# Optimization experiments

Hardware: AMD Instinct MI355X
Metric: run time of the kernel (lower is better)

## Reference

```python
import jax, jax.numpy as jnp
import numpy as np

N = 50000   # nodes
E = 800000  # edges
IN_DIM = 512
HID = 256   # total hidden (4 heads x 64)
HEADS = 4
OUT_DIM = 256
NEG_SLOPE = 0.2


def setup_inputs() -> dict:
    key = jax.random.key(0)
    ks = jax.random.split(key, 16)
    s = 0.05
    d = {
        "feats": jax.random.normal(ks[0], (N, IN_DIM), jnp.float32),
        "src": jax.random.randint(ks[1], (E,), 0, N, jnp.int32),
        "dst": jax.random.randint(ks[2], (E,), 0, N, jnp.int32),
        # layer 0: in 512 -> 4 heads x 64
        "W0": jax.random.normal(ks[3], (IN_DIM, HID), jnp.float32) * s,
        "al0": jax.random.normal(ks[4], (HEADS, HID // HEADS), jnp.float32) * s,
        "ar0": jax.random.normal(ks[5], (HEADS, HID // HEADS), jnp.float32) * s,
        "b0": jnp.zeros((HID,), jnp.float32),
        # layer 1: in 256 -> 4 heads x 64
        "W1": jax.random.normal(ks[6], (HID, HID), jnp.float32) * s,
        "al1": jax.random.normal(ks[7], (HEADS, HID // HEADS), jnp.float32) * s,
        "ar1": jax.random.normal(ks[8], (HEADS, HID // HEADS), jnp.float32) * s,
        "b1": jnp.zeros((HID,), jnp.float32),
        # layer 2: in 256 -> 1 head x 256, no activation
        "W2": jax.random.normal(ks[9], (HID, OUT_DIM), jnp.float32) * s,
        "al2": jax.random.normal(ks[10], (1, OUT_DIM), jnp.float32) * s,
        "ar2": jax.random.normal(ks[11], (1, OUT_DIM), jnp.float32) * s,
        "b2": jnp.zeros((OUT_DIM,), jnp.float32),
    }
    return d


def gat_conv(h, src, dst, W, al, ar, b, act):
    """DGL-style GATConv (no dropout, no residual). Returns [N, H, D]."""
    H, D = al.shape
    feat = (h @ W).reshape(-1, H, D)                       # [N,H,D]
    el = jnp.einsum('nhd,hd->nh', feat, al)                # [N,H]
    er = jnp.einsum('nhd,hd->nh', feat, ar)                # [N,H]
    e = jax.nn.leaky_relu(el[src] + er[dst], NEG_SLOPE)    # [E,H]
    # edge softmax over incoming edges per destination node
    m = jax.ops.segment_max(e, dst, num_segments=N)        # [N,H]
    ex = jnp.exp(e - m[dst])                               # [E,H]
    s = jax.ops.segment_sum(ex, dst, num_segments=N)       # [N,H]
    alpha = ex / s[dst]                                    # [E,H]
    msg = jax.ops.segment_sum(alpha[:, :, None] * feat[src], dst, num_segments=N)  # [N,H,D]
    out = msg + b.reshape(1, H, D)
    return act(out) if act is not None else out


def reference(feats, src, dst, W0, al0, ar0, b0, W1, al1, ar1, b1, W2, al2, ar2, b2):
    h = gat_conv(feats, src, dst, W0, al0, ar0, b0, jax.nn.relu)
    h = h.reshape(h.shape[0], -1)                          # flatten heads
    h = gat_conv(h, src, dst, W1, al1, ar1, b1, jax.nn.relu)
    h = h.reshape(h.shape[0], -1)
    h = gat_conv(h, src, dst, W2, al2, ar2, b2, None)
    h = h.mean(axis=1)                                     # last layer: mean over (single) head
    return h
```

## Files before the change

### kernel.cpp

```cpp
#include <hip/hip_runtime.h>
#include <hip/hip_bf16.h>
#include <math.h>


#define HID 256

typedef __attribute__((ext_vector_type(8))) __bf16 bf16x8;
typedef __attribute__((ext_vector_type(4))) __bf16 bf16x4;
typedef __attribute__((ext_vector_type(8))) _Float16 half8;
typedef __attribute__((ext_vector_type(4))) _Float16 half4;
typedef __attribute__((ext_vector_type(4))) float floatx4;

__device__ __forceinline__ void gl_lds16(const void* g, void* l) {
    __builtin_amdgcn_global_load_lds(
        (const __attribute__((address_space(1))) void*)g,
        (__attribute__((address_space(3))) void*)l, 16, 0, 0);
}


__global__ void hist_kernel(const int* __restrict__ dst, int* __restrict__ cnt, int E) {
    int e = blockIdx.x * blockDim.x + threadIdx.x;
    if (e < E) atomicAdd(&cnt[dst[e]], 1);
}

__global__ __launch_bounds__(256) void scan1_kernel(const int* __restrict__ cnt,
                                                    int* __restrict__ bsum, int n) {
    __shared__ int w[4];
    int t = threadIdx.x;
    int i = blockIdx.x * 256 + t;
    int c = (i < n) ? cnt[i] : 0;
    int acc = c;
#pragma unroll
    for (int off = 32; off > 0; off >>= 1) acc += __shfl_xor(acc, off);
    if ((t & 63) == 0) w[t >> 6] = acc;
    __syncthreads();
    if (t == 0) bsum[blockIdx.x] = w[0] + w[1] + w[2] + w[3];
}

__global__ __launch_bounds__(256) void scan2_kernel(const int* __restrict__ bsum,
                                                    int* __restrict__ boff, int nb) {
    __shared__ int buf[256];
    int t = threadIdx.x;
    int v = (t < nb) ? bsum[t] : 0;
    buf[t] = v;
    __syncthreads();
    for (int off = 1; off < 256; off <<= 1) {
        int x = (t >= off) ? buf[t - off] : 0;
        __syncthreads();
        buf[t] += x;
        __syncthreads();
    }
    if (t < nb) boff[t] = buf[t] - v;
}

__global__ __launch_bounds__(256) void scan3_kernel(const int* __restrict__ cnt,
                                                    const int* __restrict__ boff,
                                                    int* __restrict__ rowptr,
                                                    int* __restrict__ cursor, int n) {
    __shared__ int buf[256];
    int t = threadIdx.x;
    int i = blockIdx.x * 256 + t;
    int c = (i < n) ? cnt[i] : 0;
    buf[t] = c;
    __syncthreads();
    for (int off = 1; off < 256; off <<= 1) {
        int x = (t >= off) ? buf[t - off] : 0;
        __syncthreads();
        buf[t] += x;
        __syncthreads();
    }
    int start = boff[blockIdx.x] + buf[t] - c;
    if (i < n) {
        rowptr[i] = start;
        cursor[i] = start;
        if (i == n - 1) rowptr[n] = start + c;
    }
}

__global__ void fill_kernel(const int* __restrict__ src, const int* __restrict__ dst,
                            int* __restrict__ cursor, int* __restrict__ adj, int E) {
    int e = blockIdx.x * blockDim.x + threadIdx.x;
    if (e < E) {
        int d = dst[e];
        int pos = atomicAdd(&cursor[d], 1);
        adj[pos] = src[e];
    }
}


__device__ __forceinline__ void splitT_one(const float* W, __bf16* ht, __bf16* lt,
                                           int idx, int K) {
    int k = idx >> 8, n = idx & 255;
    float v = W[idx];
    __bf16 h = (__bf16)v;
    ht[(size_t)n * K + k] = h;
    lt[(size_t)n * K + k] = (__bf16)(v - (float)h);
}

__global__ __launch_bounds__(256) void splitT_all_kernel(
    const float* __restrict__ W0, const float* __restrict__ W1,
    const float* __restrict__ W2, __bf16* h0, __bf16* l0, __bf16* h1,
    __bf16* l1, __bf16* h2, __bf16* l2) {
    int i = blockIdx.x * 256 + threadIdx.x;
    const int n0 = 512 * 256, n1 = 256 * 256;
    if (i < n0) splitT_one(W0, h0, l0, i, 512);
    else if (i < n0 + n1) splitT_one(W1, h1, l1, i - n0, 256);
    else if (i < n0 + 2 * n1) splitT_one(W2, h2, l2, i - n0 - n1, 256);
}


template <bool SPLITA>
__global__ __launch_bounds__(256, 2) void gemm_mfma_kernel(
    const float* __restrict__ Af, const __bf16* __restrict__ Ah,
    const __bf16* __restrict__ Al, const __bf16* __restrict__ Bht,
    const __bf16* __restrict__ Blt, _Float16* __restrict__ C,
    const float* __restrict__ al, const float* __restrict__ ar,
    float* __restrict__ el, float* __restrict__ er, int M, int K, int H) {
    __shared__ __bf16 sAh[128 * 32];
    __shared__ __bf16 sAl[128 * 32];
    __shared__ __bf16 sBh[128 * 32];
    __shared__ __bf16 sBl[128 * 32];

    int t = threadIdx.x;
    int wave = t >> 6, lane = t & 63;
    int wr = wave >> 1, wc = wave & 1;
    int quad = lane >> 4, m16 = lane & 15;

    int rowA0 = blockIdx.y * 128;
    int rowB0 = blockIdx.x * 128;

    int sr = t >> 2;
    int ke = (t & 3) * 8;
    int ldso = t * 8;
    int srow = t >> 1;
    int kb = (t & 1) * 16;

    size_t ar0 = 0, ar1 = 0, af0 = 0;
    if (SPLITA) {
        af0 = (size_t)min(rowA0 + srow, M - 1) * K + kb;
    } else {
        ar0 = (size_t)min(rowA0 + sr, M - 1) * K;
        ar1 = (size_t)min(rowA0 + sr + 64, M - 1) * K;
    }
    size_t br0 = (size_t)(rowB0 + sr) * K;
    size_t br1 = (size_t)(rowB0 + sr + 64) * K;

    floatx4 acc[4][4];
    floatx4 z = {0.f, 0.f, 0.f, 0.f};
#pragma unroll
    for (int i = 0; i < 4; i++)
#pragma unroll
        for (int j = 0; j < 4; j++) acc[i][j] = z;

    int nk = K >> 5;
    for (int kt = 0; kt < nk; kt++) {
        int k0s = (kt << 5) + ke;
        gl_lds16(Bht + br0 + k0s, &sBh[ldso]);
        gl_lds16(Bht + br1 + k0s, &sBh[2048 + ldso]);
        gl_lds16(Blt + br0 + k0s, &sBl[ldso]);
        gl_lds16(Blt + br1 + k0s, &sBl[2048 + ldso]);
        if (SPLITA) {
            const float* ap = Af + af0 + (kt << 5);
            float4 v0 = ((const float4*)ap)[0];
            float4 v1 = ((const float4*)ap)[1];
            float4 v2 = ((const float4*)ap)[2];
            float4 v3 = ((const float4*)ap)[3];
            float vv[16] = {v0.x, v0.y, v0.z, v0.w, v1.x, v1.y, v1.z, v1.w,
                            v2.x, v2.y, v2.z, v2.w, v3.x, v3.y, v3.z, v3.w};
            bf16x8 h0, h1, l0, l1;
#pragma unroll
            for (int c = 0; c < 8; c++) {
                __bf16 hv = (__bf16)vv[c];
                h0[c] = hv;
                l0[c] = (__bf16)(vv[c] - (float)hv);
                __bf16 hv2 = (__bf16)vv[8 + c];
                h1[c] = hv2;
                l1[c] = (__bf16)(vv[8 + c] - (float)hv2);
            }
            int so = srow * 32 + kb;
            *(bf16x8*)&sAh[so] = h0;
            *(bf16x8*)&sAh[so + 8] = h1;
            *(bf16x8*)&sAl[so] = l0;
            *(bf16x8*)&sAl[so + 8] = l1;
        } else {
            gl_lds16(Ah + ar0 + k0s, &sAh[ldso]);
            gl_lds16(Ah + ar1 + k0s, &sAh[2048 + ldso]);
            gl_lds16(Al + ar0 + k0s, &sAl[ldso]);
            gl_lds16(Al + ar1 + k0s, &sAl[2048 + ldso]);
        }
        __syncthreads();

        bf16x8 fah[4], fal[4], fbh[4], fbl[4];
#pragma unroll
        for (int i = 0; i < 4; i++) {
            int off = (wr * 64 + i * 16 + m16) * 32 + quad * 8;
            fah[i] = *(const bf16x8*)&sAh[off];
            fal[i] = *(const bf16x8*)&sAl[off];
        }
#pragma unroll
        for (int j = 0; j < 4; j++) {
            int off = (wc * 64 + j * 16 + m16) * 32 + quad * 8;
            fbh[j] = *(const bf16x8*)&sBh[off];
            fbl[j] = *(const bf16x8*)&sBl[off];
        }
#pragma unroll
        for (int i = 0; i < 4; i++)
#pragma unroll
            for (int j = 0; j < 4; j++) {
                acc[i][j] = __builtin_amdgcn_mfma_f32_16x16x32_bf16(fah[i], fbh[j], acc[i][j], 0, 0, 0);
                acc[i][j] = __builtin_amdgcn_mfma_f32_16x16x32_bf16(fah[i], fbl[j], acc[i][j], 0, 0, 0);
                acc[i][j] = __builtin_amdgcn_mfma_f32_16x16x32_bf16(fal[i], fbh[j], acc[i][j], 0, 0, 0);
            }
        __syncthreads();
    }

#pragma unroll
    for (int i = 0; i < 4; i++) {
        int rowb = rowA0 + wr * 64 + i * 16 + quad * 4;
#pragma unroll
        for (int j = 0; j < 4; j++) {
            int col = rowB0 + wc * 64 + j * 16 + m16;
#pragma unroll
            for (int r = 0; r < 4; r++) {
                int row = rowb + r;
                if (row < M) C[(size_t)row * HID + col] = (_Float16)acc[i][j][r];
            }
        }
    }

    float alv[4], arv[4];
#pragma unroll
    for (int j = 0; j < 4; j++) {
        int col = rowB0 + wc * 64 + j * 16 + m16;
        alv[j] = al[col];
        arv[j] = ar[col];
    }
    int h = ((rowB0 + wc * 64) >> 6) & (H - 1);
#pragma unroll
    for (int i = 0; i < 4; i++) {
        int rowb = rowA0 + wr * 64 + i * 16 + quad * 4;
#pragma unroll
        for (int r = 0; r < 4; r++) {
            float pe = acc[i][0][r] * alv[0] + acc[i][1][r] * alv[1] +
                       acc[i][2][r] * alv[2] + acc[i][3][r] * alv[3];
            float pr = acc[i][0][r] * arv[0] + acc[i][1][r] * arv[1] +
                       acc[i][2][r] * arv[2] + acc[i][3][r] * arv[3];
#pragma unroll
            for (int off = 1; off < 16; off <<= 1) {
                pe += __shfl_xor(pe, off);
                pr += __shfl_xor(pr, off);
            }
            int row = rowb + r;
            if (m16 == 0 && row < M) {
                if (H == 4) {
                    el[row * 4 + h] = pe;
                    er[row * 4 + h] = pr;
                } else {
                    atomicAdd(&el[row], pe);
                    atomicAdd(&er[row], pr);
                }
            }
        }
    }
}


__global__ __launch_bounds__(256) void gemm_kernel(const float* __restrict__ A,
                                                   const float* __restrict__ B,
                                                   _Float16* __restrict__ C,
                                                   int M, int K, int Nn) {
    __shared__ float As[16][128];
    __shared__ float Bs[16][128];

    int t = threadIdx.x;
    int tx = t & 15, ty = t >> 4;
    int arow = t >> 1;
    int acol = (t & 1) * 8;
    int brow = t >> 4;
    int bcol = (t & 15) * 8;

    int gArow = blockIdx.y * 128 + arow;
    const float* aPtr = A + (size_t)gArow * K + acol;
    const float* bPtr = B + (size_t)brow * Nn + blockIdx.x * 128 + bcol;

    float acc[8][8];
#pragma unroll
    for (int i = 0; i < 8; i++)
#pragma unroll
        for (int j = 0; j < 8; j++) acc[i][j] = 0.f;

    bool aok = (gArow < M);
    int nk = K >> 4;
    for (int kt = 0; kt < nk; kt++) {
        int k0 = kt << 4;
        float4 av0 = make_float4(0.f, 0.f, 0.f, 0.f), av1 = av0;
        if (aok) {
            av0 = *(const float4*)(aPtr + k0);
            av1 = *(const float4*)(aPtr + k0 + 4);
        }
        float4 bv0 = *(const float4*)(bPtr + (size_t)k0 * Nn);
        float4 bv1 = *(const float4*)(bPtr + (size_t)k0 * Nn + 4);

        As[acol + 0][arow] = av0.x;
        As[acol + 1][arow] = av0.y;
        As[acol + 2][arow] = av0.z;
        As[acol + 3][arow] = av0.w;
        As[acol + 4][arow] = av1.x;
        As[acol + 5][arow] = av1.y;
        As[acol + 6][arow] = av1.z;
        As[acol + 7][arow] = av1.w;
        *(float4*)&Bs[brow][bcol] = bv0;
        *(float4*)&Bs[brow][bcol + 4] = bv1;
        __syncthreads();

#pragma unroll
        for (int kk = 0; kk < 16; kk++) {
            float4 a0 = *(const float4*)&As[kk][ty * 4];
            float4 a1 = *(const float4*)&As[kk][64 + ty * 4];
            float4 b0 = *(const float4*)&Bs[kk][tx * 4];
            float4 b1 = *(const float4*)&Bs[kk][64 + tx * 4];
            float a[8] = {a0.x, a0.y, a0.z, a0.w, a1.x, a1.y, a1.z, a1.w};
            float b[8] = {b0.x, b0.y, b0.z, b0.w, b1.x, b1.y, b1.z, b1.w};
#pragma unroll
            for (int i = 0; i < 8; i++)
#pragma unroll
                for (int j = 0; j < 8; j++) acc[i][j] = fmaf(a[i], b[j], acc[i][j]);
        }
        __syncthreads();
    }

    int c0 = blockIdx.x * 128 + tx * 4;
#pragma unroll
    for (int half = 0; half < 2; half++) {
#pragma unroll
        for (int i = 0; i < 4; i++) {
            int r = blockIdx.y * 128 + half * 64 + ty * 4 + i;
            if (r < M) {
                _Float16* cp = C + (size_t)r * Nn + c0;
                int ai = half * 4 + i;
#pragma unroll
                for (int j = 0; j < 4; j++) {
                    cp[j] = (_Float16)acc[ai][j];
                    cp[64 + j] = (_Float16)acc[ai][4 + j];
                }
            }
        }
    }
}


__global__ __launch_bounds__(256) void elr_kernel(const _Float16* __restrict__ feat,
                                                  const float* __restrict__ al,
                                                  const float* __restrict__ ar,
                                                  float* __restrict__ el,
                                                  float* __restrict__ er, int H) {
    int n = blockIdx.x, t = threadIdx.x;
    float f = (float)feat[(size_t)n * HID + t];
    float a = f * al[t];
    float b = f * ar[t];
#pragma unroll
    for (int off = 32; off > 0; off >>= 1) {
        a += __shfl_xor(a, off);
        b += __shfl_xor(b, off);
    }
    __shared__ float pa[4], pb[4];
    int wave = t >> 6, lane = t & 63;
    if (lane == 0) { pa[wave] = a; pb[wave] = b; }
    __syncthreads();
    if (H == 4) {
        if (t < 4) {
            el[n * 4 + t] = pa[t];
            er[n * 4 + t] = pb[t];
        }
    } else {
        if (t == 0) {
            el[n] = pa[0] + pa[1] + pa[2] + pa[3];
            er[n] = pb[0] + pb[1] + pb[2] + pb[3];
        }
    }
}


template <int H, bool RELU, bool WF32, bool WSPLIT>
__global__ __launch_bounds__(256) void agg_tpl(
    const _Float16* __restrict__ feat, const float* __restrict__ el,
    const float* __restrict__ er, const int* __restrict__ rowptr,
    const int* __restrict__ adj, const float* __restrict__ bias,
    float* __restrict__ outf, __bf16* __restrict__ oh, __bf16* __restrict__ ol,
    int N) {
    int wave = threadIdx.x >> 6, lane = threadIdx.x & 63;
    int v = blockIdx.x * 4 + wave;
    if (v >= N) return;
    int row0 = rowptr[v];
    int deg = rowptr[v + 1] - row0;

    int l32 = lane & 31;
    int half = lane >> 5;
    int hd = (H == 4) ? (l32 >> 3) : 0;
    int d0 = l32 * 8;

    float o[8];
    if (deg > 0) {
        float er_h = (H == 4) ? er[v * 4 + hd] : er[v];
        const int* adjr = adj + row0;

        float a[8];
#pragma unroll
        for (int j = 0; j < 8; j++) a[j] = 0.f;
        float sl = 0.f;

        int e = 0;
        for (; e + 16 <= deg; e += 16) {
            int u[8];
            half8 f[8];
            float elv[8];
#pragma unroll
            for (int q = 0; q < 8; q++) u[q] = adjr[e + q * 2 + half];
#pragma unroll
            for (int q = 0; q < 8; q++)
                f[q] = *(const half8*)&feat[(size_t)u[q] * HID + d0];
#pragma unroll
            for (int q = 0; q < 8; q++)
                elv[q] = (H == 4) ? el[u[q] * 4 + hd] : el[u[q]];
#pragma unroll
            for (int q = 0; q < 8; q++) {
                float sc = elv[q] + er_h;
                sc = (sc > 0.f) ? sc : 0.2f * sc;
                float ex = __expf(sc);
                sl += ex;
#pragma unroll
                for (int j = 0; j < 8; j++) a[j] = fmaf(ex, (float)f[q][j], a[j]);
            }
        }
        for (; e + 8 <= deg; e += 8) {
            int u[4];
            half8 f[4];
            float elv[4];
#pragma unroll
            for (int q = 0; q < 4; q++) u[q] = adjr[e + q * 2 + half];
#pragma unroll
            for (int q = 0; q < 4; q++)
                f[q] = *(const half8*)&feat[(size_t)u[q] * HID + d0];
#pragma unroll
            for (int q = 0; q < 4; q++)
                elv[q] = (H == 4) ? el[u[q] * 4 + hd] : el[u[q]];
#pragma unroll
            for (int q = 0; q < 4; q++) {
                float sc = elv[q] + er_h;
                sc = (sc > 0.f) ? sc : 0.2f * sc;
                float ex = __expf(sc);
                sl += ex;
#pragma unroll
                for (int j = 0; j < 8; j++) a[j] = fmaf(ex, (float)f[q][j], a[j]);
            }
        }
        for (; e < deg; e += 2) {
            int ee = e + half;
            bool act = ee < deg;
            int es = act ? ee : (deg - 1);
            int u = adjr[es];
            float elvq = (H == 4) ? el[u * 4 + hd] : el[u];
            half8 f = *(const half8*)&feat[(size_t)u * HID + d0];
            float sc = elvq + er_h;
            sc = (sc > 0.f) ? sc : 0.2f * sc;
            float ex = act ? __expf(sc) : 0.f;
            sl += ex;
#pragma unroll
            for (int j = 0; j < 8; j++) a[j] = fmaf(ex, (float)f[j], a[j]);
        }

#pragma unroll
        for (int j = 0; j < 8; j++) a[j] += __shfl_xor(a[j], 32);
        sl += __shfl_xor(sl, 32);
        float inv = 1.f / sl;

#pragma unroll
        for (int j = 0; j < 8; j++) {
            o[j] = fmaf(a[j], inv, bias[d0 + j]);
            if (RELU) o[j] = fmaxf(o[j], 0.f);
        }
    } else {
#pragma unroll
        for (int j = 0; j < 8; j++) {
            o[j] = bias[d0 + j];
            if (RELU) o[j] = fmaxf(o[j], 0.f);
        }
    }

    if (half == 0) {
        size_t base = (size_t)v * HID + d0;
        if (WF32) {
            *(float4*)&outf[base] = make_float4(o[0], o[1], o[2], o[3]);
            *(float4*)&outf[base + 4] = make_float4(o[4], o[5], o[6], o[7]);
        }
        if (WSPLIT) {
            bf16x8 hh, ll;
#pragma unroll
            for (int j = 0; j < 8; j++) {
                __bf16 hv = (__bf16)o[j];
                hh[j] = hv;
                ll[j] = (__bf16)(o[j] - (float)hv);
            }
            *(bf16x8*)&oh[base] = hh;
            *(bf16x8*)&ol[base] = ll;
        }
    }
}


extern "C" void kernel_launch(void* const* d_in, const int* in_sizes, int n_in,
                              void* d_out, int out_size, void* d_ws, size_t ws_size,
                              hipStream_t stream) {
    const float* feats = (const float*)d_in[0];
    const int* src = (const int*)d_in[1];
    const int* dst = (const int*)d_in[2];
    const float* W0 = (const float*)d_in[3];
    const float* al0 = (const float*)d_in[4];
    const float* ar0 = (const float*)d_in[5];
    const float* b0 = (const float*)d_in[6];
    const float* W1 = (const float*)d_in[7];
    const float* al1 = (const float*)d_in[8];
    const float* ar1 = (const float*)d_in[9];
    const float* b1 = (const float*)d_in[10];
    const float* W2 = (const float*)d_in[11];
    const float* al2 = (const float*)d_in[12];
    const float* ar2 = (const float*)d_in[13];
    const float* b2 = (const float*)d_in[14];
    float* out = (float*)d_out;

    const int IN_DIM = 512;
    const int N = in_sizes[0] / IN_DIM;
    const int E = in_sizes[1];

    char* ws = (char*)d_ws;
    size_t off = 0;
    auto alloc = [&](size_t bytes) -> void* {
        void* p = ws + off;
        off = (off + bytes + 255) & ~(size_t)255;
        return p;
    };
    _Float16* featbuf = (_Float16*)alloc((size_t)N * HID * sizeof(_Float16));
    float* el = (float*)alloc((size_t)N * 4 * sizeof(float));
    float* er = (float*)alloc((size_t)N * 4 * sizeof(float));
    int* cnt = (int*)alloc((size_t)N * sizeof(int));
    int* rowptr = (int*)alloc((size_t)(N + 1) * sizeof(int));
    int* cursor = (int*)alloc((size_t)N * sizeof(int));
    int* adj = (int*)alloc((size_t)E * sizeof(int));
    int nscanb = (N + 255) / 256;
    int* bsum = (int*)alloc((size_t)nscanb * sizeof(int));
    int* boff = (int*)alloc((size_t)nscanb * sizeof(int));
    __bf16* Ah = (__bf16*)alloc((size_t)N * HID * sizeof(__bf16));
    __bf16* Al = (__bf16*)alloc((size_t)N * HID * sizeof(__bf16));
    __bf16* Bht0 = (__bf16*)alloc((size_t)512 * HID * sizeof(__bf16));
    __bf16* Blt0 = (__bf16*)alloc((size_t)512 * HID * sizeof(__bf16));
    __bf16* Bht1 = (__bf16*)alloc((size_t)256 * HID * sizeof(__bf16));
    __bf16* Blt1 = (__bf16*)alloc((size_t)256 * HID * sizeof(__bf16));
    __bf16* Bht2 = (__bf16*)alloc((size_t)256 * HID * sizeof(__bf16));
    __bf16* Blt2 = (__bf16*)alloc((size_t)256 * HID * sizeof(__bf16));
    bool use_mfma = (off <= ws_size);

    hipMemsetAsync(cnt, 0, (size_t)N * sizeof(int), stream);
    hist_kernel<<<(E + 255) / 256, 256, 0, stream>>>(dst, cnt, E);
    scan1_kernel<<<nscanb, 256, 0, stream>>>(cnt, bsum, N);
    scan2_kernel<<<1, 256, 0, stream>>>(bsum, boff, nscanb);
    scan3_kernel<<<nscanb, 256, 0, stream>>>(cnt, boff, rowptr, cursor, N);
    fill_kernel<<<(E + 255) / 256, 256, 0, stream>>>(src, dst, cursor, adj, E);

    dim3 ggrid(HID / 128, (N + 127) / 128);
    int aggb = (N + 3) / 4;

    if (use_mfma) {
        splitT_all_kernel<<<(512 * 256 + 2 * 256 * 256) / 256, 256, 0, stream>>>(
            W0, W1, W2, Bht0, Blt0, Bht1, Blt1, Bht2, Blt2);

        gemm_mfma_kernel<true><<<ggrid, 256, 0, stream>>>(
            feats, nullptr, nullptr, Bht0, Blt0, featbuf, al0, ar0, el, er, N, 512, 4);
        agg_tpl<4, true, false, true><<<aggb, 256, 0, stream>>>(
            featbuf, el, er, rowptr, adj, b0, nullptr, Ah, Al, N);

        gemm_mfma_kernel<false><<<ggrid, 256, 0, stream>>>(
            nullptr, Ah, Al, Bht1, Blt1, featbuf, al1, ar1, el, er, N, 256, 4);
        agg_tpl<4, true, false, true><<<aggb, 256, 0, stream>>>(
            featbuf, el, er, rowptr, adj, b1, nullptr, Ah, Al, N);

        hipMemsetAsync(el, 0, (size_t)N * 8 * sizeof(float), stream);
        gemm_mfma_kernel<false><<<ggrid, 256, 0, stream>>>(
            nullptr, Ah, Al, Bht2, Blt2, featbuf, al2, ar2, el, er, N, 256, 1);
        agg_tpl<1, false, true, false><<<aggb, 256, 0, stream>>>(
            featbuf, el, er, rowptr, adj, b2, out, nullptr, nullptr, N);
    } else {
        gemm_kernel<<<ggrid, 256, 0, stream>>>(feats, W0, featbuf, N, 512, HID);
        elr_kernel<<<N, 256, 0, stream>>>(featbuf, al0, ar0, el, er, 4);
        agg_tpl<4, true, true, false><<<aggb, 256, 0, stream>>>(
            featbuf, el, er, rowptr, adj, b0, out, nullptr, nullptr, N);

        gemm_kernel<<<ggrid, 256, 0, stream>>>(out, W1, featbuf, N, 256, HID);
        elr_kernel<<<N, 256, 0, stream>>>(featbuf, al1, ar1, el, er, 4);
        agg_tpl<4, true, true, false><<<aggb, 256, 0, stream>>>(
            featbuf, el, er, rowptr, adj, b1, out, nullptr, nullptr, N);

        gemm_kernel<<<ggrid, 256, 0, stream>>>(out, W2, featbuf, N, 256, HID);
        elr_kernel<<<N, 256, 0, stream>>>(featbuf, al2, ar2, el, er, 1);
        agg_tpl<1, false, true, false><<<aggb, 256, 0, stream>>>(
            featbuf, el, er, rowptr, adj, b2, out, nullptr, nullptr, N);
    }
}
```

Baseline: 614.3 us.

## Double-buffer GEMM LDS tiles and XOR-swizzle shared layout

The split-bf16 MFMA GEMM now uses two LDS buffers, issuing global-to-LDS loads (and fp32 A loads) for the next k-tile before computing on the current one. The A split into high and low parts is written after the MFMAs, and one barrier per iteration is removed. An XOR swizzle on the k-chunk index is applied to both the LDS writes and the fragment reads to reduce bank conflicts. LDS use doubles to 64KB per block, which may limit the two-blocks-per-CU occupancy target.

```diff
diff --git a/kernel.cpp b/kernel.cpp
--- a/kernel.cpp
+++ b/kernel.cpp
@@ -116,10 +116,10 @@
     const __bf16* __restrict__ Blt, _Float16* __restrict__ C,
     const float* __restrict__ al, const float* __restrict__ ar,
     float* __restrict__ el, float* __restrict__ er, int M, int K, int H) {
-    __shared__ __bf16 sAh[128 * 32];
-    __shared__ __bf16 sAl[128 * 32];
-    __shared__ __bf16 sBh[128 * 32];
-    __shared__ __bf16 sBl[128 * 32];
+    __shared__ __bf16 sAh[2][4096];
+    __shared__ __bf16 sAl[2][4096];
+    __shared__ __bf16 sBh[2][4096];
+    __shared__ __bf16 sBl[2][4096];
 
     int t = threadIdx.x;
     int wave = t >> 6, lane = t & 63;
@@ -130,10 +130,14 @@
     int rowB0 = blockIdx.x * 128;
 
     int sr = t >> 2;
-    int ke = (t & 3) * 8;
+    int ke = ((t & 3) ^ ((t >> 3) & 3)) * 8;
     int ldso = t * 8;
     int srow = t >> 1;
     int kb = (t & 1) * 16;
+    int s0 = (t & 1) * 2;
+    int ssw = (srow >> 1) & 3;
+    int soA = srow * 32 + (s0 ^ ssw) * 8;
+    int soB = srow * 32 + ((s0 + 1) ^ ssw) * 8;
 
     size_t ar0 = 0, ar1 = 0, af0 = 0;
     if (SPLITA) {
@@ -145,6 +149,8 @@
     size_t br0 = (size_t)(rowB0 + sr) * K;
     size_t br1 = (size_t)(rowB0 + sr + 64) * K;
 
+    int qsw = (quad ^ ((m16 >> 1) & 3)) * 8;
+
     floatx4 acc[4][4];
     floatx4 z = {0.f, 0.f, 0.f, 0.f};
 #pragma unroll
@@ -153,14 +159,14 @@
         for (int j = 0; j < 4; j++) acc[i][j] = z;
 
     int nk = K >> 5;
-    for (int kt = 0; kt < nk; kt++) {
-        int k0s = (kt << 5) + ke;
-        gl_lds16(Bht + br0 + k0s, &sBh[ldso]);
-        gl_lds16(Bht + br1 + k0s, &sBh[2048 + ldso]);
-        gl_lds16(Blt + br0 + k0s, &sBl[ldso]);
-        gl_lds16(Blt + br1 + k0s, &sBl[2048 + ldso]);
+
+    {
+        gl_lds16(Bht + br0 + ke, &sBh[0][ldso]);
+        gl_lds16(Bht + br1 + ke, &sBh[0][2048 + ldso]);
+        gl_lds16(Blt + br0 + ke, &sBl[0][ldso]);
+        gl_lds16(Blt + br1 + ke, &sBl[0][2048 + ldso]);
         if (SPLITA) {
-            const float* ap = Af + af0 + (kt << 5);
+            const float* ap = Af + af0;
             float4 v0 = ((const float4*)ap)[0];
             float4 v1 = ((const float4*)ap)[1];
             float4 v2 = ((const float4*)ap)[2];
@@ -177,32 +183,60 @@
                 h1[c] = hv2;
                 l1[c] = (__bf16)(vv[8 + c] - (float)hv2);
             }
-            int so = srow * 32 + kb;
-            *(bf16x8*)&sAh[so] = h0;
-            *(bf16x8*)&sAh[so + 8] = h1;
-            *(bf16x8*)&sAl[so] = l0;
-            *(bf16x8*)&sAl[so + 8] = l1;
+            *(bf16x8*)&sAh[0][soA] = h0;
+            *(bf16x8*)&sAh[0][soB] = h1;
+            *(bf16x8*)&sAl[0][soA] = l0;
+            *(bf16x8*)&sAl[0][soB] = l1;
         } else {
-            gl_lds16(Ah + ar0 + k0s, &sAh[ldso]);
-            gl_lds16(Ah + ar1 + k0s, &sAh[2048 + ldso]);
-            gl_lds16(Al + ar0 + k0s, &sAl[ldso]);
-            gl_lds16(Al + ar1 + k0s, &sAl[2048 + ldso]);
-        }
-        __syncthreads();
+            gl_lds16(Ah + ar0 + ke, &sAh[0][ldso]);
+            gl_lds16(Ah + ar1 + ke, &sAh[0][2048 + ldso]);
+            gl_lds16(Al + ar0 + ke, &sAl[0][ldso]);
+            gl_lds16(Al + ar1 + ke, &sAl[0][2048 + ldso]);
+        }
+    }
+    __syncthreads();
+
+    int cur = 0;
+    for (int kt = 0; kt < nk; kt++) {
+        int nxt = cur ^ 1;
+        bool have = (kt + 1 < nk);
+
+        float4 v0, v1, v2, v3;
+        if (have) {
+            int k1 = (kt + 1) << 5;
+            int k0s = k1 + ke;
+            gl_lds16(Bht + br0 + k0s, &sBh[nxt][ldso]);
+            gl_lds16(Bht + br1 + k0s, &sBh[nxt][2048 + ldso]);
+            gl_lds16(Blt + br0 + k0s, &sBl[nxt][ldso]);
+            gl_lds16(Blt + br1 + k0s, &sBl[nxt][2048 + ldso]);
+            if (SPLITA) {
+                const float* ap = Af + af0 + k1;
+                v0 = ((const float4*)ap)[0];
+                v1 = ((const float4*)ap)[1];
+                v2 = ((const float4*)ap)[2];
+                v3 = ((const float4*)ap)[3];
+            } else {
+                gl_lds16(Ah + ar0 + k0s, &sAh[nxt][ldso]);
+                gl_lds16(Ah + ar1 + k0s, &sAh[nxt][2048 + ldso]);
+                gl_lds16(Al + ar0 + k0s, &sAl[nxt][ldso]);
+                gl_lds16(Al + ar1 + k0s, &sAl[nxt][2048 + ldso]);
+            }
+        }
 
         bf16x8 fah[4], fal[4], fbh[4], fbl[4];
 #pragma unroll
         for (int i = 0; i < 4; i++) {
-            int off = (wr * 64 + i * 16 + m16) * 32 + quad * 8;
-            fah[i] = *(const bf16x8*)&sAh[off];
-            fal[i] = *(const bf16x8*)&sAl[off];
+            int off = (wr * 64 + i * 16 + m16) * 32 + qsw;
+            fah[i] = *(const bf16x8*)&sAh[cur][off];
+            fal[i] = *(const bf16x8*)&sAl[cur][off];
         }
 #pragma unroll
         for (int j = 0; j < 4; j++) {
-            int off = (wc * 64 + j * 16 + m16) * 32 + quad * 8;
-            fbh[j] = *(const bf16x8*)&sBh[off];
-            fbl[j] = *(const bf16x8*)&sBl[off];
-        }
+            int off = (wc * 64 + j * 16 + m16) * 32 + qsw;
+            fbh[j] = *(const bf16x8*)&sBh[cur][off];
+            fbl[j] = *(const bf16x8*)&sBl[cur][off];
+        }
+
 #pragma unroll
         for (int i = 0; i < 4; i++)
 #pragma unroll
@@ -211,7 +245,28 @@
                 acc[i][j] = __builtin_amdgcn_mfma_f32_16x16x32_bf16(fah[i], fbl[j], acc[i][j], 0, 0, 0);
                 acc[i][j] = __builtin_amdgcn_mfma_f32_16x16x32_bf16(fal[i], fbh[j], acc[i][j], 0, 0, 0);
             }
+
+        if (SPLITA && have) {
+            float vv[16] = {v0.x, v0.y, v0.z, v0.w, v1.x, v1.y, v1.z, v1.w,
+                            v2.x, v2.y, v2.z, v2.w, v3.x, v3.y, v3.z, v3.w};
+            bf16x8 h0, h1, l0, l1;
+#pragma unroll
+            for (int c = 0; c < 8; c++) {
+                __bf16 hv = (__bf16)vv[c];
+                h0[c] = hv;
+                l0[c] = (__bf16)(vv[c] - (float)hv);
+                __bf16 hv2 = (__bf16)vv[8 + c];
+                h1[c] = hv2;
+                l1[c] = (__bf16)(vv[8 + c] - (float)hv2);
+            }
+            *(bf16x8*)&sAh[nxt][soA] = h0;
+            *(bf16x8*)&sAh[nxt][soB] = h1;
+            *(bf16x8*)&sAl[nxt][soA] = l0;
+            *(bf16x8*)&sAl[nxt][soB] = l1;
+        }
+
         __syncthreads();
+        cur = nxt;
     }
 
 #pragma unroll
```

Result: no change. 616.7 us (+0.4%).

## Load GEMM MFMA fragments directly from global memory, dropping LDS staging

Applied to the files above, without the earlier changes.

The GEMM kernel no longer stages A and B tiles through shared memory with global_load_lds and barriers. Each lane now loads its MFMA fragments straight from global memory into registers, and the launch bound for the non-split variant goes up to 3 blocks per CU. This removes the LDS round trip and the __syncthreads calls, but each tile is now fetched redundantly by the waves that share it (A by 2 waves, B by 2 waves), which depends on L1/L2 to absorb the repeated loads. The 16-byte loads strided across rows may also coalesce poorly.

```diff
diff --git a/kernel.cpp b/kernel.cpp
--- a/kernel.cpp
+++ b/kernel.cpp
@@ -10,12 +10,6 @@
 typedef __attribute__((ext_vector_type(8))) _Float16 half8;
 typedef __attribute__((ext_vector_type(4))) _Float16 half4;
 typedef __attribute__((ext_vector_type(4))) float floatx4;
-
-__device__ __forceinline__ void gl_lds16(const void* g, void* l) {
-    __builtin_amdgcn_global_load_lds(
-        (const __attribute__((address_space(1))) void*)g,
-        (__attribute__((address_space(3))) void*)l, 16, 0, 0);
-}
 
 
 __global__ void hist_kernel(const int* __restrict__ dst, int* __restrict__ cnt, int E) {
@@ -110,17 +104,12 @@
 
 
 template <bool SPLITA>
-__global__ __launch_bounds__(256, 2) void gemm_mfma_kernel(
+__global__ __launch_bounds__(256, SPLITA ? 2 : 3) void gemm_reg_kernel(
     const float* __restrict__ Af, const __bf16* __restrict__ Ah,
     const __bf16* __restrict__ Al, const __bf16* __restrict__ Bht,
     const __bf16* __restrict__ Blt, _Float16* __restrict__ C,
     const float* __restrict__ al, const float* __restrict__ ar,
     float* __restrict__ el, float* __restrict__ er, int M, int K, int H) {
-    __shared__ __bf16 sAh[128 * 32];
-    __shared__ __bf16 sAl[128 * 32];
-    __shared__ __bf16 sBh[128 * 32];
-    __shared__ __bf16 sBl[128 * 32];
-
     int t = threadIdx.x;
     int wave = t >> 6, lane = t & 63;
     int wr = wave >> 1, wc = wave & 1;
@@ -129,21 +118,21 @@
     int rowA0 = blockIdx.y * 128;
     int rowB0 = blockIdx.x * 128;
 
-    int sr = t >> 2;
-    int ke = (t & 3) * 8;
-    int ldso = t * 8;
-    int srow = t >> 1;
-    int kb = (t & 1) * 16;
-
-    size_t ar0 = 0, ar1 = 0, af0 = 0;
-    if (SPLITA) {
-        af0 = (size_t)min(rowA0 + srow, M - 1) * K + kb;
-    } else {
-        ar0 = (size_t)min(rowA0 + sr, M - 1) * K;
-        ar1 = (size_t)min(rowA0 + sr + 64, M - 1) * K;
-    }
-    size_t br0 = (size_t)(rowB0 + sr) * K;
-    size_t br1 = (size_t)(rowB0 + sr + 64) * K;
+    size_t aoff0, aoff1, aoff2, aoff3;
+    {
+        int r0 = min(rowA0 + wr * 64 + 0 * 16 + m16, M - 1);
+        int r1 = min(rowA0 + wr * 64 + 1 * 16 + m16, M - 1);
+        int r2 = min(rowA0 + wr * 64 + 2 * 16 + m16, M - 1);
+        int r3 = min(rowA0 + wr * 64 + 3 * 16 + m16, M - 1);
+        aoff0 = (size_t)r0 * K + quad * 8;
+        aoff1 = (size_t)r1 * K + quad * 8;
+        aoff2 = (size_t)r2 * K + quad * 8;
+        aoff3 = (size_t)r3 * K + quad * 8;
+    }
+    size_t boff0 = (size_t)(rowB0 + wc * 64 + 0 * 16 + m16) * K + quad * 8;
+    size_t boff1 = (size_t)(rowB0 + wc * 64 + 1 * 16 + m16) * K + quad * 8;
+    size_t boff2 = (size_t)(rowB0 + wc * 64 + 2 * 16 + m16) * K + quad * 8;
+    size_t boff3 = (size_t)(rowB0 + wc * 64 + 3 * 16 + m16) * K + quad * 8;
 
     floatx4 acc[4][4];
     floatx4 z = {0.f, 0.f, 0.f, 0.f};
@@ -154,55 +143,46 @@
 
     int nk = K >> 5;
     for (int kt = 0; kt < nk; kt++) {
-        int k0s = (kt << 5) + ke;
-        gl_lds16(Bht + br0 + k0s, &sBh[ldso]);
-        gl_lds16(Bht + br1 + k0s, &sBh[2048 + ldso]);
-        gl_lds16(Blt + br0 + k0s, &sBl[ldso]);
-        gl_lds16(Blt + br1 + k0s, &sBl[2048 + ldso]);
+        int k0 = kt << 5;
+        bf16x8 fah[4], fal[4], fbh[4], fbl[4];
+
         if (SPLITA) {
-            const float* ap = Af + af0 + (kt << 5);
-            float4 v0 = ((const float4*)ap)[0];
-            float4 v1 = ((const float4*)ap)[1];
-            float4 v2 = ((const float4*)ap)[2];
-            float4 v3 = ((const float4*)ap)[3];
-            float vv[16] = {v0.x, v0.y, v0.z, v0.w, v1.x, v1.y, v1.z, v1.w,
-                            v2.x, v2.y, v2.z, v2.w, v3.x, v3.y, v3.z, v3.w};
-            bf16x8 h0, h1, l0, l1;
-#pragma unroll
-            for (int c = 0; c < 8; c++) {
-                __bf16 hv = (__bf16)vv[c];
-                h0[c] = hv;
-                l0[c] = (__bf16)(vv[c] - (float)hv);
-                __bf16 hv2 = (__bf16)vv[8 + c];
-                h1[c] = hv2;
-                l1[c] = (__bf16)(vv[8 + c] - (float)hv2);
-            }
-            int so = srow * 32 + kb;
-            *(bf16x8*)&sAh[so] = h0;
-            *(bf16x8*)&sAh[so + 8] = h1;
-            *(bf16x8*)&sAl[so] = l0;
-            *(bf16x8*)&sAl[so + 8] = l1;
+            size_t ao[4] = {aoff0, aoff1, aoff2, aoff3};
+#pragma unroll
+            for (int i = 0; i < 4; i++) {
+                const float* ap = Af + ao[i] + k0;
+                float4 v0 = ((const float4*)ap)[0];
+                float4 v1 = ((const float4*)ap)[1];
+                float vv[8] = {v0.x, v0.y, v0.z, v0.w, v1.x, v1.y, v1.z, v1.w};
+                bf16x8 h, l;
+#pragma unroll
+                for (int c = 0; c < 8; c++) {
+                    __bf16 hv = (__bf16)vv[c];
+                    h[c] = hv;
+                    l[c] = (__bf16)(vv[c] - (float)hv);
+                }
+                fah[i] = h;
+                fal[i] = l;
+            }
         } else {
-            gl_lds16(Ah + ar0 + k0s, &sAh[ldso]);
-            gl_lds16(Ah + ar1 + k0s, &sAh[2048 + ldso]);
-            gl_lds16(Al + ar0 + k0s, &sAl[ldso]);
-            gl_lds16(Al + ar1 + k0s, &sAl[2048 + ldso]);
-        }
-        __syncthreads();
-
-        bf16x8 fah[4], fal[4], fbh[4], fbl[4];
-#pragma unroll
-        for (int i = 0; i < 4; i++) {
-            int off = (wr * 64 + i * 16 + m16) * 32 + quad * 8;
-            fah[i] = *(const bf16x8*)&sAh[off];
-            fal[i] = *(const bf16x8*)&sAl[off];
-        }
-#pragma unroll
-        for (int j = 0; j < 4; j++) {
-            int off = (wc * 64 + j * 16 + m16) * 32 + quad * 8;
-            fbh[j] = *(const bf16x8*)&sBh[off];
-            fbl[j] = *(const bf16x8*)&sBl[off];
-        }
+            fah[0] = *(const bf16x8*)(Ah + aoff0 + k0);
+            fah[1] = *(const bf16x8*)(Ah + aoff1 + k0);
+            fah[2] = *(const bf16x8*)(Ah + aoff2 + k0);
+            fah[3] = *(const bf16x8*)(Ah + aoff3 + k0);
+            fal[0] = *(const bf16x8*)(Al + aoff0 + k0);
+            fal[1] = *(const bf16x8*)(Al + aoff1 + k0);
+            fal[2] = *(const bf16x8*)(Al + aoff2 + k0);
+            fal[3] = *(const bf16x8*)(Al + aoff3 + k0);
+        }
+        fbh[0] = *(const bf16x8*)(Bht + boff0 + k0);
+        fbh[1] = *(const bf16x8*)(Bht + boff1 + k0);
+        fbh[2] = *(const bf16x8*)(Bht + boff2 + k0);
+        fbh[3] = *(const bf16x8*)(Bht + boff3 + k0);
+        fbl[0] = *(const bf16x8*)(Blt + boff0 + k0);
+        fbl[1] = *(const bf16x8*)(Blt + boff1 + k0);
+        fbl[2] = *(const bf16x8*)(Blt + boff2 + k0);
+        fbl[3] = *(const bf16x8*)(Blt + boff3 + k0);
+
 #pragma unroll
         for (int i = 0; i < 4; i++)
 #pragma unroll
@@ -211,7 +191,6 @@
                 acc[i][j] = __builtin_amdgcn_mfma_f32_16x16x32_bf16(fah[i], fbl[j], acc[i][j], 0, 0, 0);
                 acc[i][j] = __builtin_amdgcn_mfma_f32_16x16x32_bf16(fal[i], fbh[j], acc[i][j], 0, 0, 0);
             }
-        __syncthreads();
     }
 
 #pragma unroll
@@ -573,18 +552,18 @@
         splitT_all_kernel<<<(512 * 256 + 2 * 256 * 256) / 256, 256, 0, stream>>>(
             W0, W1, W2, Bht0, Blt0, Bht1, Blt1, Bht2, Blt2);
 
-        gemm_mfma_kernel<true><<<ggrid, 256, 0, stream>>>(
+        gemm_reg_kernel<true><<<ggrid, 256, 0, stream>>>(
             feats, nullptr, nullptr, Bht0, Blt0, featbuf, al0, ar0, el, er, N, 512, 4);
         agg_tpl<4, true, false, true><<<aggb, 256, 0, stream>>>(
             featbuf, el, er, rowptr, adj, b0, nullptr, Ah, Al, N);
 
-        gemm_mfma_kernel<false><<<ggrid, 256, 0, stream>>>(
+        gemm_reg_kernel<false><<<ggrid, 256, 0, stream>>>(
             nullptr, Ah, Al, Bht1, Blt1, featbuf, al1, ar1, el, er, N, 256, 4);
         agg_tpl<4, true, false, true><<<aggb, 256, 0, stream>>>(
             featbuf, el, er, rowptr, adj, b1, nullptr, Ah, Al, N);
 
         hipMemsetAsync(el, 0, (size_t)N * 8 * sizeof(float), stream);
-        gemm_mfma_kernel<false><<<ggrid, 256, 0, stream>>>(
+        gemm_reg_kernel<false><<<ggrid, 256, 0, stream>>>(
             nullptr, Ah, Al, Bht2, Blt2, featbuf, al2, ar2, el, er, N, 256, 1);
         agg_tpl<1, false, true, false><<<aggb, 256, 0, stream>>>(
             featbuf, el, er, rowptr, adj, b2, out, nullptr, nullptr, N);
```

After: 750.7 us. 22.2% more time.
